# Kernel tuning notes

Measured on AMD Instinct MI355X. Metric: run time of the kernel, lower is better.

Reference implementation:

```python
import jax, jax.numpy as jnp
import numpy as np

N_NODES = 100000
N_EDGES = 1_600_000
F_IN, HID, N_CLS = 128, 64, 32
NEG_SLOPE = 0.2  # PyG GATv2Conv default


def _segment_softmax(scores, seg, num_segments):
    # numerically stable softmax over edges grouped by destination node
    m = jax.ops.segment_max(scores, seg, num_segments=num_segments)
    ex = jnp.exp(scores - m[seg])
    s = jax.ops.segment_sum(ex, seg, num_segments=num_segments)
    return ex / (s[seg] + 1e-16)


def _gatv2_layer(x, src, dst, Wl, bl, Wr, br, att, bias, num_nodes):
    xl = x @ Wl + bl              # source transform  [N, C]
    xr = x @ Wr + br              # target transform  [N, C]
    # per-edge GATv2 attention logit: a . leaky_relu(xl_j + xr_i)
    e = jax.nn.leaky_relu(xl[src] + xr[dst], NEG_SLOPE) @ att  # [E]
    alpha = _segment_softmax(e, dst, num_nodes)                 # [E]
    out = jax.ops.segment_sum(alpha[:, None] * xl[src], dst, num_segments=num_nodes)
    return out + bias


def _add_self_loops(edge_index, n):
    loops = jnp.arange(n, dtype=edge_index.dtype)
    return jnp.concatenate([edge_index, jnp.stack([loops, loops])], axis=1)


def setup_inputs() -> dict:
    key = jax.random.key(0)
    ks = jax.random.split(key, 8)
    s1 = 1.0 / np.sqrt(F_IN)
    s2 = 1.0 / np.sqrt(HID)
    return {
        "x": jax.random.normal(ks[0], (N_NODES, F_IN), jnp.float32),
        "edge_index": jax.random.randint(ks[1], (2, N_EDGES), 0, N_NODES, jnp.int64),
        "W1l": jax.random.normal(ks[2], (F_IN, HID), jnp.float32) * s1,
        "b1l": jnp.zeros((HID,), jnp.float32),
        "W1r": jax.random.normal(ks[3], (F_IN, HID), jnp.float32) * s1,
        "b1r": jnp.zeros((HID,), jnp.float32),
        "att1": jax.random.normal(ks[4], (HID,), jnp.float32) * s2,
        "bias1": jnp.zeros((HID,), jnp.float32),
        "W2l": jax.random.normal(ks[5], (HID, N_CLS), jnp.float32) * s2,
        "b2l": jnp.zeros((N_CLS,), jnp.float32),
        "W2r": jax.random.normal(ks[6], (HID, N_CLS), jnp.float32) * s2,
        "b2r": jnp.zeros((N_CLS,), jnp.float32),
        "att2": jax.random.normal(ks[7], (N_CLS,), jnp.float32) / np.sqrt(N_CLS),
        "bias2": jnp.zeros((N_CLS,), jnp.float32),
    }


def reference(x, edge_index, W1l, b1l, W1r, b1r, att1, bias1,
              W2l, b2l, W2r, b2r, att2, bias2):
    n = x.shape[0]
    ei = _add_self_loops(edge_index, n)
    src, dst = ei[0], ei[1]
    h = jax.nn.relu(_gatv2_layer(x, src, dst, W1l, b1l, W1r, b1r, att1, bias1, n))
    # F.dropout(training=False) is identity in eval mode
    out = _gatv2_layer(h, src, dst, W2l, b2l, W2r, b2r, att2, bias2, n)
    return out
```

## Files before the change

### kernel.cpp

```cpp
#include <hip/hip_runtime.h>
#include <hip/hip_fp16.h>
#include <math.h>

#define F_IN 128
#define HID 64
#define NCLS 32
#define NEG 0.2f
#define NBKT 256
#define CHUNK 8192

using bf8 = __attribute__((ext_vector_type(8))) short;
using f4v = __attribute__((ext_vector_type(4))) float;
typedef _Float16 hv2 __attribute__((ext_vector_type(2)));

__device__ __forceinline__ void f4fma(float4& a, float s, const float4& w) {
    a.x = fmaf(s, w.x, a.x);
    a.y = fmaf(s, w.y, a.y);
    a.z = fmaf(s, w.z, a.z);
    a.w = fmaf(s, w.w, a.w);
}
__device__ __forceinline__ unsigned short f2bf(float f) {
    unsigned u = __float_as_uint(f);
    return (unsigned short)((u + 0x7FFFu + ((u >> 16) & 1u)) >> 16);
}
__device__ __forceinline__ unsigned short f2h(float f) {
    return __half_as_ushort(__float2half(f));
}
__device__ __forceinline__ float h2f(unsigned short u) {
    return __half2float(__ushort_as_half(u));
}
__device__ __forceinline__ unsigned pkaddabs(unsigned a, unsigned b) {
    hv2 r = __builtin_bit_cast(hv2, a) + __builtin_bit_cast(hv2, b);
    return __builtin_bit_cast(unsigned, r) & 0x7FFF7FFFu;
}
__device__ __forceinline__ float fdot2(unsigned a, unsigned b, float c) {
    return __builtin_amdgcn_fdot2(__builtin_bit_cast(hv2, a),
                                  __builtin_bit_cast(hv2, b), c, false);
}
__device__ __forceinline__ float h2lo(unsigned a) {
    return (float)__builtin_bit_cast(hv2, a).x;
}
__device__ __forceinline__ float h2hi(unsigned a) {
    return (float)__builtin_bit_cast(hv2, a).y;
}
template <int CTRL>
__device__ __forceinline__ float dpp_add(float v) {
    int t = __builtin_amdgcn_update_dpp(0, __float_as_int(v), CTRL, 0xf, 0xf, true);
    return v + __int_as_float(t);
}


__global__ __launch_bounds__(256) void zeroBuckets(int* __restrict__ bucketSize, int BK) {
    int i = blockIdx.x * 256 + threadIdx.x;
    if (i < BK) bucketSize[i] = 0;
}

__global__ __launch_bounds__(256) void bucketHist(const int* __restrict__ ei,
                                                  int Eorig, int Etot,
                                                  int* __restrict__ bucketSize, int BK) {
    __shared__ int h[512];
    int t = threadIdx.x;
    for (int j = t; j < BK; j += 256) h[j] = 0;
    __syncthreads();
    int base = blockIdx.x * CHUNK;
    int end = base + CHUNK < Etot ? base + CHUNK : Etot;
    for (int i = base + t; i < end; i += 256) {
        int dst = i < Eorig ? ei[Eorig + i] : i - Eorig;
        atomicAdd(&h[dst >> 8], 1);
    }
    __syncthreads();
    for (int j = t; j < BK; j += 256)
        if (h[j]) atomicAdd(&bucketSize[j], h[j]);
}

__global__ __launch_bounds__(256) void bucketScan(const int* __restrict__ bucketSize,
                                                  int* __restrict__ bucketStart,
                                                  int* __restrict__ bucketCursor,
                                                  int BK, int Etot) {
    __shared__ int sd[256];
    int t = threadIdx.x;
    int v0 = (2 * t     < BK) ? bucketSize[2 * t]     : 0;
    int v1 = (2 * t + 1 < BK) ? bucketSize[2 * t + 1] : 0;
    int ts = v0 + v1;
    sd[t] = ts;
    __syncthreads();
    for (int off = 1; off < 256; off <<= 1) {
        int x = (t >= off) ? sd[t - off] : 0;
        __syncthreads();
        sd[t] += x;
        __syncthreads();
    }
    int excl = sd[t] - ts;
    if (2 * t < BK)     { bucketStart[2 * t] = excl;          bucketCursor[2 * t] = excl; }
    if (2 * t + 1 < BK) { bucketStart[2 * t + 1] = excl + v0; bucketCursor[2 * t + 1] = excl + v0; }
    if (t == 255) bucketStart[BK] = Etot;
}

__global__ __launch_bounds__(256) void bucketScatter(const int* __restrict__ ei,
                                                     int Eorig, int Etot,
                                                     int* __restrict__ bucketCursor,
                                                     int2* __restrict__ pairs, int BK) {
    __shared__ int h[512], lbase[512], hcur[512];
    int t = threadIdx.x;
    for (int j = t; j < BK; j += 256) { h[j] = 0; hcur[j] = 0; }
    __syncthreads();
    int base = blockIdx.x * CHUNK;
    int end = base + CHUNK < Etot ? base + CHUNK : Etot;
    for (int i = base + t; i < end; i += 256) {
        int dst = i < Eorig ? ei[Eorig + i] : i - Eorig;
        atomicAdd(&h[dst >> 8], 1);
    }
    __syncthreads();
    for (int j = t; j < BK; j += 256)
        lbase[j] = h[j] ? atomicAdd(&bucketCursor[j], h[j]) : 0;
    __syncthreads();
    for (int i = base + t; i < end; i += 256) {
        int src, dst;
        if (i < Eorig) { src = ei[i]; dst = ei[Eorig + i]; }
        else           { src = dst = i - Eorig; }
        int b = dst >> 8;
        int off = atomicAdd(&hcur[b], 1);
        pairs[lbase[b] + off] = make_int2(src, dst);
    }
}

__global__ __launch_bounds__(256) void bucketCSR(const int2* __restrict__ pairs,
                                                 const int* __restrict__ bucketStart,
                                                 int* __restrict__ rowstart,
                                                 int* __restrict__ cnt,
                                                 int* __restrict__ srclist, int N) {
    __shared__ int c[256], cur[256];
    int t = threadIdx.x;
    int b = blockIdx.x;
    int lo = b * NBKT;
    int eb = bucketStart[b], ee = bucketStart[b + 1];
    c[t] = 0;
    __syncthreads();
    for (int i = eb + t; i < ee; i += 256)
        atomicAdd(&c[pairs[i].y - lo], 1);
    __syncthreads();
    cur[t] = c[t];
    __syncthreads();
    for (int off = 1; off < 256; off <<= 1) {
        int x = (t >= off) ? cur[t - off] : 0;
        __syncthreads();
        cur[t] += x;
        __syncthreads();
    }
    int excl = cur[t] - c[t];
    int node = lo + t;
    if (node < N) { rowstart[node] = eb + excl; cnt[node] = c[t]; }
    __syncthreads();
    cur[t] = excl;
    __syncthreads();
    for (int i = eb + t; i < ee; i += 256) {
        int2 pr = pairs[i];
        int pos = atomicAdd(&cur[pr.y - lo], 1);
        srclist[eb + pos] = pr.x;
    }
}

__global__ __launch_bounds__(256) void prepW(const float* __restrict__ Wl,
                                             const float* __restrict__ Wr,
                                             const float* __restrict__ att1,
                                             const float* __restrict__ att2,
                                             uint4* __restrict__ wfrag,
                                             unsigned short* __restrict__ att1h,
                                             unsigned short* __restrict__ att2h) {
    int e = blockIdx.x * 256 + threadIdx.x;
    if (e >= 2048) {
        int i = e - 2048;
        if (i < HID) att1h[i] = f2h(att1[i]);
        else if (i < HID + NCLS) att2h[i - HID] = f2h(att2[i - HID]);
        return;
    }
    int lane = e & 63;
    int kt = (e >> 6) & 3;
    int ct = (e >> 8) & 3;
    int mat = e >> 10;
    const float* W = mat ? Wr : Wl;
    int k0 = kt * 32 + (lane >> 4) * 8;
    int c = ct * 16 + (lane & 15);
    unsigned short h[8];
#pragma unroll
    for (int j = 0; j < 8; j++) h[j] = f2bf(W[(k0 + j) * HID + c]);
    wfrag[e] = *(uint4*)h;
}

__global__ __launch_bounds__(256) void transform1(const float* __restrict__ x,
                                                  const uint4* __restrict__ wfrag,
                                                  const float* __restrict__ bl,
                                                  const float* __restrict__ br,
                                                  const float* __restrict__ att,
                                                  unsigned short* __restrict__ xlh,
                                                  unsigned short* __restrict__ xrh,
                                                  float* __restrict__ sl, int N) {
    __shared__ uint4 sw[2048];
    int t = threadIdx.x;
#pragma unroll
    for (int j = 0; j < 8; j++) sw[t + j * 256] = wfrag[t + j * 256];
    __syncthreads();

    int w = t >> 6, lane = t & 63;
    int nb = blockIdx.x * 64 + w * 16;
    int m = lane & 15, quad = lane >> 4;

    int arow = nb + m; if (arow >= N) arow = N - 1;
    const float* xrow = x + (size_t)arow * F_IN + quad * 8;
    bf8 afr[4];
#pragma unroll
    for (int kt = 0; kt < 4; kt++) {
        float4 lo = *(const float4*)(xrow + kt * 32);
        float4 hi = *(const float4*)(xrow + kt * 32 + 4);
        unsigned short hh[8];
        hh[0] = f2bf(lo.x); hh[1] = f2bf(lo.y); hh[2] = f2bf(lo.z); hh[3] = f2bf(lo.w);
        hh[4] = f2bf(hi.x); hh[5] = f2bf(hi.y); hh[6] = f2bf(hi.z); hh[7] = f2bf(hi.w);
        afr[kt] = *(bf8*)hh;
    }

    float am[4];
#pragma unroll
    for (int ct = 0; ct < 4; ct++) am[ct] = att[ct * 16 + m];
    float slp[4] = {0.f, 0.f, 0.f, 0.f};

#pragma unroll
    for (int mat = 0; mat < 2; mat++) {
        const float* bias = mat ? br : bl;
#pragma unroll
        for (int ct = 0; ct < 4; ct++) {
            f4v acc = {0.f, 0.f, 0.f, 0.f};
#pragma unroll
            for (int kt = 0; kt < 4; kt++) {
                bf8 bfr = *(bf8*)&sw[((mat * 4 + ct) * 4 + kt) * 64 + lane];
                acc = __builtin_amdgcn_mfma_f32_16x16x32_bf16(afr[kt], bfr, acc, 0, 0, 0);
            }
            int ch = ct * 16 + m;
            float bv = bias[ch];
#pragma unroll
            for (int reg = 0; reg < 4; reg++) {
                int node = nb + quad * 4 + reg;
                float o = acc[reg] + bv;
                if (mat) {
                    if (node < N) xrh[(size_t)node * HID + ch] = f2h(o);
                } else {
                    unsigned short hb = f2h(o);
                    slp[reg] = fmaf(am[ct], h2f(hb), slp[reg]);
                    if (node < N) xlh[(size_t)node * HID + ch] = hb;
                }
            }
        }
    }
#pragma unroll
    for (int o2 = 1; o2 < 16; o2 <<= 1) {
#pragma unroll
        for (int reg = 0; reg < 4; reg++) slp[reg] += __shfl_xor(slp[reg], o2, 64);
    }
    if (m == 0) {
#pragma unroll
        for (int reg = 0; reg < 4; reg++) {
            int node = nb + quad * 4 + reg;
            if (node < N) sl[node] = 0.6f * slp[reg];
        }
    }
}

__global__ __launch_bounds__(256) void transform2(const float* __restrict__ h,
                                                  const float* __restrict__ Wl,
                                                  const float* __restrict__ bl,
                                                  const float* __restrict__ Wr,
                                                  const float* __restrict__ br,
                                                  const float* __restrict__ att,
                                                  unsigned short* __restrict__ xlh,
                                                  unsigned short* __restrict__ xrh,
                                                  float* __restrict__ sl, int N) {
    __shared__ float sWl[HID * NCLS];
    __shared__ float sWr[HID * NCLS];
    __shared__ float sx[128][68];
    int t = threadIdx.x;
    int nb = blockIdx.x * 128;

#pragma unroll
    for (int j = 0; j < 2; j++) {
        int f = t + j * 256;
        ((float4*)sWl)[f] = ((const float4*)Wl)[f];
        ((float4*)sWr)[f] = ((const float4*)Wr)[f];
    }
    int maxf = (N - nb) * 16;
#pragma unroll
    for (int j = 0; j < 8; j++) {
        int f = t + j * 256;
        int node = f >> 4, kc = f & 15;
        float4 v = {0.f, 0.f, 0.f, 0.f};
        if (f < maxf) v = ((const float4*)(h + (size_t)nb * HID))[f];
        v.x = fmaxf(v.x, 0.f);
        v.y = fmaxf(v.y, 0.f);
        v.z = fmaxf(v.z, 0.f);
        v.w = fmaxf(v.w, 0.f);
        *(float4*)&sx[node][kc * 4] = v;
    }
    __syncthreads();

    int c4 = (t & 7) * 4;
    int slot = t >> 3;
    float4 bl4 = *(const float4*)(bl + c4);
    float4 br4 = *(const float4*)(br + c4);
    float4 at4 = *(const float4*)(att + c4);
    float4 accl[4] = {bl4, bl4, bl4, bl4};
    float4 accr[4] = {br4, br4, br4, br4};

#pragma unroll 4
    for (int k4 = 0; k4 < HID / 4; k4++) {
        int k = k4 * 4;
        float4 wl0 = *(const float4*)&sWl[(k + 0) * NCLS + c4];
        float4 wl1 = *(const float4*)&sWl[(k + 1) * NCLS + c4];
        float4 wl2 = *(const float4*)&sWl[(k + 2) * NCLS + c4];
        float4 wl3 = *(const float4*)&sWl[(k + 3) * NCLS + c4];
        float4 wr0 = *(const float4*)&sWr[(k + 0) * NCLS + c4];
        float4 wr1 = *(const float4*)&sWr[(k + 1) * NCLS + c4];
        float4 wr2 = *(const float4*)&sWr[(k + 2) * NCLS + c4];
        float4 wr3 = *(const float4*)&sWr[(k + 3) * NCLS + c4];
#pragma unroll
        for (int j = 0; j < 4; j++) {
            float4 xv = *(const float4*)&sx[slot + j * 32][k];
            f4fma(accl[j], xv.x, wl0); f4fma(accr[j], xv.x, wr0);
            f4fma(accl[j], xv.y, wl1); f4fma(accr[j], xv.y, wr1);
            f4fma(accl[j], xv.z, wl2); f4fma(accr[j], xv.z, wr2);
            f4fma(accl[j], xv.w, wl3); f4fma(accr[j], xv.w, wr3);
        }
    }
#pragma unroll
    for (int j = 0; j < 4; j++) {
        ushort4 o;
        o.x = f2h(accl[j].x); o.y = f2h(accl[j].y);
        o.z = f2h(accl[j].z); o.w = f2h(accl[j].w);
        ushort4 orr;
        orr.x = f2h(accr[j].x); orr.y = f2h(accr[j].y);
        orr.z = f2h(accr[j].z); orr.w = f2h(accr[j].w);
        float slpj = fmaf(at4.x, h2f(o.x),
                     fmaf(at4.y, h2f(o.y),
                     fmaf(at4.z, h2f(o.z), at4.w * h2f(o.w))));
        slpj += __shfl_xor(slpj, 1, 64);
        slpj += __shfl_xor(slpj, 2, 64);
        slpj += __shfl_xor(slpj, 4, 64);
        int g = nb + slot + j * 32;
        if (g < N) {
            *(ushort4*)(xlh + (size_t)g * NCLS + c4) = o;
            *(ushort4*)(xrh + (size_t)g * NCLS + c4) = orr;
            if ((t & 7) == 0) sl[g] = 0.6f * slpj;
        }
    }
}

#define AGG_BATCH(EIDX, WEXPR)                                        \
    {                                                                 \
        int src = __shfl(srcv, (EIDX), 64);                           \
        float tA = __shfl(slvA, (EIDX), 64);                          \
        unsigned vp[NH];                                              \
        const unsigned short* rowp = xlh + (unsigned)src * C + cb0;   \
        if (NH == 4) *(uint4*)vp = *(const uint4*)rowp;               \
        else         *(uint2*)vp = *(const uint2*)rowp;               \
        float pa = 0.f;                                               \
        _Pragma("unroll")                                             \
        for (int j = 0; j < NH; j++)                                  \
            pa = fdot2(pkaddabs(vp[j], xrp[j]), atp[j], pa);          \
        pa = dpp_add<0x128>(pa);                                      \
        pa += __shfl_xor(pa, 16, 64);                                 \
        pa += __shfl_xor(pa, 32, 64);                                 \
        float wgt = (WEXPR);                                          \
        s += wgt;                                                     \
        _Pragma("unroll")                                             \
        for (int j = 0; j < NH; j++) {                                \
            acc[2 * j]     = fmaf(wgt, h2lo(vp[j]), acc[2 * j]);      \
            acc[2 * j + 1] = fmaf(wgt, h2hi(vp[j]), acc[2 * j + 1]);  \
        }                                                             \
    }

template <int C>
__global__ __launch_bounds__(256) void fusedAggD(const unsigned short* __restrict__ xlh,
                                                 const unsigned short* __restrict__ xrh,
                                                 const unsigned short* __restrict__ atth,
                                                 const float* __restrict__ sl,
                                                 const int* __restrict__ rowstart,
                                                 const int* __restrict__ cnt,
                                                 const int* __restrict__ srclist,
                                                 const float* __restrict__ bias,
                                                 float* __restrict__ out, int N) {
    constexpr int CH = C / 8;
    constexpr int NH = CH / 2;
    int wid = threadIdx.x >> 6;
    int lane = threadIdx.x & 63;
    int n = blockIdx.x * 4 + wid;
    if (n >= N) return;

    int slot = lane & 7;
    int pos  = lane >> 3;
    int cb0  = pos * CH;

    unsigned xrp[NH], atp[NH];
    if (NH == 4) {
        *(uint4*)xrp = *(const uint4*)(xrh + (size_t)n * C + cb0);
        *(uint4*)atp = *(const uint4*)(atth + cb0);
    } else {
        *(uint2*)xrp = *(const uint2*)(xrh + (size_t)n * C + cb0);
        *(uint2*)atp = *(const uint2*)(atth + cb0);
    }

    float srp = 0.f;
#pragma unroll
    for (int j = 0; j < NH; j++) srp = fdot2(xrp[j], atp[j], srp);
    srp = dpp_add<0x128>(srp);
    srp += __shfl_xor(srp, 16, 64);
    srp += __shfl_xor(srp, 32, 64);
    float sr06 = 0.6f * srp;

    int row = rowstart[n];
    int deg = cnt[n];

    float s = 0.f;
    float acc[CH];
#pragma unroll
    for (int c = 0; c < CH; c++) acc[c] = 0.f;

    for (int cb = 0; cb < deg; cb += 64) {
        int len = deg - cb; if (len > 64) len = 64;
        int li = lane < len ? lane : len - 1;
        int srcv = srclist[row + cb + li];
        float slvA = sl[srcv] + sr06;
        int nfull = len >> 3, rem = len & 7;
#pragma unroll 2
        for (int b = 0; b < nfull; b++) {
            AGG_BATCH(b * 8 + slot, __expf(fmaf(0.4f, pa, tA)))
        }
        if (rem) {
            AGG_BATCH(nfull * 8 + slot,
                      (slot < rem) ? __expf(fmaf(0.4f, pa, tA)) : 0.f)
        }
    }
#pragma unroll
    for (int c = 0; c < CH; c++) {
        acc[c] = dpp_add<0xB1>(acc[c]);
        acc[c] = dpp_add<0x4E>(acc[c]);
        acc[c] = dpp_add<0x141>(acc[c]);
    }
    s = dpp_add<0xB1>(s);
    s = dpp_add<0x4E>(s);
    s = dpp_add<0x141>(s);

    if (slot == 0) {
        float inv = 1.f / (s + 1e-16f);
        float o8[CH];
        float bi[CH];
        if (NH == 4) {
            *(float4*)&bi[0] = *(const float4*)(bias + cb0);
            *(float4*)&bi[4] = *(const float4*)(bias + cb0 + 4);
        } else {
            *(float4*)&bi[0] = *(const float4*)(bias + cb0);
        }
#pragma unroll
        for (int c = 0; c < CH; c++) o8[c] = fmaf(acc[c], inv, bi[c]);
        if (NH == 4) {
            *(float4*)(out + (size_t)n * C + cb0)     = *(float4*)&o8[0];
            *(float4*)(out + (size_t)n * C + cb0 + 4) = *(float4*)&o8[4];
        } else {
            *(float4*)(out + (size_t)n * C + cb0) = *(float4*)&o8[0];
        }
    }
}

extern "C" void kernel_launch(void* const* d_in, const int* in_sizes, int n_in,
                              void* d_out, int out_size, void* d_ws, size_t ws_size,
                              hipStream_t stream) {
    const float* x     = (const float*)d_in[0];
    const int*   ei    = (const int*)d_in[1];
    const float* W1l   = (const float*)d_in[2];
    const float* b1l   = (const float*)d_in[3];
    const float* W1r   = (const float*)d_in[4];
    const float* b1r   = (const float*)d_in[5];
    const float* att1  = (const float*)d_in[6];
    const float* bias1 = (const float*)d_in[7];
    const float* W2l   = (const float*)d_in[8];
    const float* b2l   = (const float*)d_in[9];
    const float* W2r   = (const float*)d_in[10];
    const float* b2r   = (const float*)d_in[11];
    const float* att2  = (const float*)d_in[12];
    const float* bias2 = (const float*)d_in[13];
    float* out = (float*)d_out;

    int N     = in_sizes[0] / F_IN;
    int Eorig = in_sizes[1] / 2;
    int Etot  = Eorig + N;
    int BK    = (N + NBKT - 1) / NBKT;

    char* p = (char*)d_ws;
    auto alloc = [&](size_t bytes) { void* r = (void*)p; p += (bytes + 255) & ~(size_t)255; return r; };
    unsigned short* xl1h = (unsigned short*)alloc((size_t)N * HID * 2);
    unsigned short* xr1h = (unsigned short*)alloc((size_t)N * HID * 2);
    float* h       = (float*)alloc((size_t)N * HID * 4);
    unsigned short* xl2h = (unsigned short*)alloc((size_t)N * NCLS * 2);
    unsigned short* xr2h = (unsigned short*)alloc((size_t)N * NCLS * 2);
    int*   cnt     = (int*)alloc((size_t)N * 4);
    int*   rowstart= (int*)alloc((size_t)N * 4);
    int*   srclist = (int*)alloc((size_t)Etot * 4);
    uint4* wfrag   = (uint4*)alloc(2048 * 16);
    float* sl1     = (float*)alloc((size_t)N * 4);
    float* sl2     = (float*)alloc((size_t)N * 4);
    unsigned short* att1h = (unsigned short*)alloc(HID * 2);
    unsigned short* att2h = (unsigned short*)alloc(NCLS * 2);
    int*   bucketSize   = (int*)alloc(520 * 4);
    int*   bucketStart  = (int*)alloc(520 * 4);
    int*   bucketCursor = (int*)alloc(520 * 4);
    int2*  pairs   = (int2*)h;

    int nChunks = (Etot + CHUNK - 1) / CHUNK;

    zeroBuckets<<<2, 256, 0, stream>>>(bucketSize, BK);
    bucketHist<<<nChunks, 256, 0, stream>>>(ei, Eorig, Etot, bucketSize, BK);
    bucketScan<<<1, 256, 0, stream>>>(bucketSize, bucketStart, bucketCursor, BK, Etot);
    bucketScatter<<<nChunks, 256, 0, stream>>>(ei, Eorig, Etot, bucketCursor, pairs, BK);
    bucketCSR<<<BK, 256, 0, stream>>>(pairs, bucketStart, rowstart, cnt, srclist, N);

    prepW<<<9, 256, 0, stream>>>(W1l, W1r, att1, att2, wfrag, att1h, att2h);
    transform1<<<(N + 63) / 64, 256, 0, stream>>>(x, wfrag, b1l, b1r, att1, xl1h, xr1h, sl1, N);
    fusedAggD<HID><<<(N + 3) / 4, 256, 0, stream>>>(xl1h, xr1h, att1h, sl1, rowstart, cnt,
                                                    srclist, bias1, h, N);

    transform2<<<(N + 127) / 128, 256, 0, stream>>>(h, W2l, b2l, W2r, b2r, att2, xl2h, xr2h, sl2, N);
    fusedAggD<NCLS><<<(N + 3) / 4, 256, 0, stream>>>(xl2h, xr2h, att2h, sl2, rowstart, cnt,
                                                     srclist, bias2, out, N);
}
```

Measured before the change: 310.7 us.

## Pack bucket pairs into one int and load edge sources directly in aggregation

Bucket scatter now stores each (src, dst) pair as a single 32-bit word, src shifted left by 8 with the low 8 bits of dst. This halves the scatter and CSR-build traffic, and relies on node ids fitting in 24 bits. The aggregation kernel drops the per-destination target score, which is a constant shift that cancels in the softmax. Each edge batch now reads srclist and sl per lane directly instead of staging a 64-edge chunk and broadcasting with shuffles. The xor-16 reduction step uses ds_swizzle instead of a generic shuffle; the trade-off is redundant same-address loads per edge slot and no max-shift in the exponent.

```diff
diff --git a/kernel.cpp b/kernel.cpp
--- a/kernel.cpp
+++ b/kernel.cpp
@@ -46,6 +46,10 @@
 template <int CTRL>
 __device__ __forceinline__ float dpp_add(float v) {
     int t = __builtin_amdgcn_update_dpp(0, __float_as_int(v), CTRL, 0xf, 0xf, true);
+    return v + __int_as_float(t);
+}
+__device__ __forceinline__ float swz16_add(float v) {
+    int t = __builtin_amdgcn_ds_swizzle(__float_as_int(v), 0x401F);
     return v + __int_as_float(t);
 }
 
@@ -99,7 +103,7 @@
 __global__ __launch_bounds__(256) void bucketScatter(const int* __restrict__ ei,
                                                      int Eorig, int Etot,
                                                      int* __restrict__ bucketCursor,
-                                                     int2* __restrict__ pairs, int BK) {
+                                                     int* __restrict__ pairs, int BK) {
     __shared__ int h[512], lbase[512], hcur[512];
     int t = threadIdx.x;
     for (int j = t; j < BK; j += 256) { h[j] = 0; hcur[j] = 0; }
@@ -120,11 +124,11 @@
         else           { src = dst = i - Eorig; }
         int b = dst >> 8;
         int off = atomicAdd(&hcur[b], 1);
-        pairs[lbase[b] + off] = make_int2(src, dst);
-    }
-}
-
-__global__ __launch_bounds__(256) void bucketCSR(const int2* __restrict__ pairs,
+        pairs[lbase[b] + off] = (src << 8) | (dst & 255);
+    }
+}
+
+__global__ __launch_bounds__(256) void bucketCSR(const int* __restrict__ pairs,
                                                  const int* __restrict__ bucketStart,
                                                  int* __restrict__ rowstart,
                                                  int* __restrict__ cnt,
@@ -137,7 +141,7 @@
     c[t] = 0;
     __syncthreads();
     for (int i = eb + t; i < ee; i += 256)
-        atomicAdd(&c[pairs[i].y - lo], 1);
+        atomicAdd(&c[pairs[i] & 255], 1);
     __syncthreads();
     cur[t] = c[t];
     __syncthreads();
@@ -154,9 +158,9 @@
     cur[t] = excl;
     __syncthreads();
     for (int i = eb + t; i < ee; i += 256) {
-        int2 pr = pairs[i];
-        int pos = atomicAdd(&cur[pr.y - lo], 1);
-        srclist[eb + pos] = pr.x;
+        int v = pairs[i];
+        int pos = atomicAdd(&cur[v & 255], 1);
+        srclist[eb + pos] = v >> 8;
     }
 }
 
@@ -351,10 +355,12 @@
     }
 }
 
-#define AGG_BATCH(EIDX, WEXPR)                                        \
+#define AGG_BATCH(EIDX, CLAMP, WEXPR)                                 \
     {                                                                 \
-        int src = __shfl(srcv, (EIDX), 64);                           \
-        float tA = __shfl(slvA, (EIDX), 64);                          \
+        int eidx = row + (EIDX);                                      \
+        if (CLAMP) eidx = min(eidx, rowend1);                         \
+        int src = srclist[eidx];                                      \
+        float tA = sl[src];                                           \
         unsigned vp[NH];                                              \
         const unsigned short* rowp = xlh + (unsigned)src * C + cb0;   \
         if (NH == 4) *(uint4*)vp = *(const uint4*)rowp;               \
@@ -364,7 +370,7 @@
         for (int j = 0; j < NH; j++)                                  \
             pa = fdot2(pkaddabs(vp[j], xrp[j]), atp[j], pa);          \
         pa = dpp_add<0x128>(pa);                                      \
-        pa += __shfl_xor(pa, 16, 64);                                 \
+        pa = swz16_add(pa);                                           \
         pa += __shfl_xor(pa, 32, 64);                                 \
         float wgt = (WEXPR);                                          \
         s += wgt;                                                     \
@@ -376,7 +382,7 @@
     }
 
 template <int C>
-__global__ __launch_bounds__(256) void fusedAggD(const unsigned short* __restrict__ xlh,
+__global__ __launch_bounds__(256) void fusedAggE(const unsigned short* __restrict__ xlh,
                                                  const unsigned short* __restrict__ xrh,
                                                  const unsigned short* __restrict__ atth,
                                                  const float* __restrict__ sl,
@@ -405,16 +411,9 @@
         *(uint2*)atp = *(const uint2*)(atth + cb0);
     }
 
-    float srp = 0.f;
-#pragma unroll
-    for (int j = 0; j < NH; j++) srp = fdot2(xrp[j], atp[j], srp);
-    srp = dpp_add<0x128>(srp);
-    srp += __shfl_xor(srp, 16, 64);
-    srp += __shfl_xor(srp, 32, 64);
-    float sr06 = 0.6f * srp;
-
     int row = rowstart[n];
     int deg = cnt[n];
+    int rowend1 = row + deg - 1;
 
     float s = 0.f;
     float acc[CH];
@@ -423,16 +422,13 @@
 
     for (int cb = 0; cb < deg; cb += 64) {
         int len = deg - cb; if (len > 64) len = 64;
-        int li = lane < len ? lane : len - 1;
-        int srcv = srclist[row + cb + li];
-        float slvA = sl[srcv] + sr06;
         int nfull = len >> 3, rem = len & 7;
 #pragma unroll 2
         for (int b = 0; b < nfull; b++) {
-            AGG_BATCH(b * 8 + slot, __expf(fmaf(0.4f, pa, tA)))
+            AGG_BATCH(cb + b * 8 + slot, false, __expf(fmaf(0.4f, pa, tA)))
         }
         if (rem) {
-            AGG_BATCH(nfull * 8 + slot,
+            AGG_BATCH(cb + nfull * 8 + slot, true,
                       (slot < rem) ? __expf(fmaf(0.4f, pa, tA)) : 0.f)
         }
     }
@@ -509,7 +505,7 @@
     int*   bucketSize   = (int*)alloc(520 * 4);
     int*   bucketStart  = (int*)alloc(520 * 4);
     int*   bucketCursor = (int*)alloc(520 * 4);
-    int2*  pairs   = (int2*)h;
+    int*   pairs   = (int*)h;
 
     int nChunks = (Etot + CHUNK - 1) / CHUNK;
 
@@ -521,10 +517,10 @@
 
     prepW<<<9, 256, 0, stream>>>(W1l, W1r, att1, att2, wfrag, att1h, att2h);
     transform1<<<(N + 63) / 64, 256, 0, stream>>>(x, wfrag, b1l, b1r, att1, xl1h, xr1h, sl1, N);
-    fusedAggD<HID><<<(N + 3) / 4, 256, 0, stream>>>(xl1h, xr1h, att1h, sl1, rowstart, cnt,
+    fusedAggE<HID><<<(N + 3) / 4, 256, 0, stream>>>(xl1h, xr1h, att1h, sl1, rowstart, cnt,
                                                     srclist, bias1, h, N);
 
     transform2<<<(N + 127) / 128, 256, 0, stream>>>(h, W2l, b2l, W2r, b2r, att2, xl2h, xr2h, sl2, N);
-    fusedAggD<NCLS><<<(N + 3) / 4, 256, 0, stream>>>(xl2h, xr2h, att2h, sl2, rowstart, cnt,
+    fusedAggE<NCLS><<<(N + 3) / 4, 256, 0, stream>>>(xl2h, xr2h, att2h, sl2, rowstart, cnt,
                                                      srclist, bias2, out, N);
 }
```

Result: slower. 319.6 us (+2.9%).
